# Performance work log

Measured on AMD Instinct MI355X. Metric: run time of the kernel, lower is better.

The kernel has to match this reference:

```python
import jax, jax.numpy as jnp
import numpy as np

B, N, D, H = 8, 1024, 1024, 16
DK = D // H


def setup_inputs() -> dict:
    key = jax.random.key(0)
    ks = jax.random.split(key, 5)
    s_in = 1.0 / np.sqrt(D)
    return {
        "x": jax.random.normal(ks[0], (B, N, D), dtype=jnp.float32),
        "w_qkv": jax.random.uniform(ks[1], (D, 3 * D), jnp.float32, -s_in, s_in),
        "b_qkv": jax.random.uniform(ks[2], (3 * D,), jnp.float32, -s_in, s_in),
        "w_proj": jax.random.uniform(ks[3], (D, D), jnp.float32, -s_in, s_in),
        "b_proj": jax.random.uniform(ks[4], (D,), jnp.float32, -s_in, s_in),
    }


def reference(x, w_qkv, b_qkv, w_proj, b_proj):
    # x: (B, N, D)
    qkv = x @ w_qkv + b_qkv                      # (B, N, 3D)
    q, k, v = jnp.split(qkv, 3, axis=-1)
    # reshape to (B, H, N, DK)
    def heads(t):
        return t.reshape(B, N, H, DK).transpose(0, 2, 1, 3)
    q, k, v = heads(q), heads(k), heads(v)
    scale = 1.0 / np.sqrt(DK).astype(np.float32)
    scores = jnp.einsum("bhnd,bhmd->bhnm", q, k) * scale  # (B, H, N, N)
    attn = jax.nn.softmax(scores, axis=-1)
    out = jnp.einsum("bhnm,bhmd->bhnd", attn, v)          # (B, H, N, DK)
    out = out.transpose(0, 2, 1, 3).reshape(B, N, D)
    return out @ w_proj + b_proj
```

## Files before the change

### kernel.cpp

```cpp
#include <hip/hip_runtime.h>
#include <hip/hip_bf16.h>


#define BB 8
#define NN 1024
#define DD 1024
#define HH 16
#define DK 64
#define TOK (BB * NN)
#define QKVN (3 * DD)

typedef __attribute__((ext_vector_type(8))) short bf16x8;
typedef __attribute__((ext_vector_type(4))) float f32x4;
typedef __attribute__((ext_vector_type(4))) short short4v;
typedef __attribute__((ext_vector_type(4))) float float4v;

static __device__ __forceinline__ short f2bf(float f) {
  union { float f; unsigned u; } v; v.f = f;
  unsigned r = (v.u + 0x7FFFu + ((v.u >> 16) & 1u)) >> 16;
  return (short)r;
}
static __device__ __forceinline__ short f2bf_rn(float f) {
  __hip_bfloat16 h(f);
  short s;
  __builtin_memcpy(&s, &h, 2);
  return s;
}
static __device__ __forceinline__ float fexp2(float x) {
#if __has_builtin(__builtin_amdgcn_exp2f)
  return __builtin_amdgcn_exp2f(x);
#else
  return __expf(x * 0.69314718056f);
#endif
}

static __device__ __forceinline__ void gload_lds16(const short* g, short* lds, int lane) {
#if __has_builtin(__builtin_amdgcn_global_load_lds)
  __builtin_amdgcn_global_load_lds((const __attribute__((address_space(1))) void*)g,
                                   (__attribute__((address_space(3))) void*)lds, 16, 0, 0);
#else
  ((bf16x8*)lds)[lane] = *(const bf16x8*)g;
#endif
}

static __device__ __forceinline__ void block_barrier() {
  asm volatile("" ::: "memory");
  __builtin_amdgcn_s_barrier();
  asm volatile("" ::: "memory");
}

__global__ __launch_bounds__(256) void cast_f32_bf16(const float* __restrict__ in,
                                                     short* __restrict__ out, long n) {
  long i = ((long)blockIdx.x * blockDim.x + threadIdx.x) * 4;
  if (i >= n) return;
  float4v v = *(const float4v*)(in + i);
  short4v o;
  o[0] = f2bf(v[0]); o[1] = f2bf(v[1]); o[2] = f2bf(v[2]); o[3] = f2bf(v[3]);
  *(short4v*)(out + i) = o;
}

__global__ __launch_bounds__(256) void transpose_cast(const float* __restrict__ in,
                                                      short* __restrict__ out,
                                                      int rows, int cols) {
  __shared__ float tile[32][33];
  int bx = blockIdx.x * 32;
  int by = blockIdx.y * 32;
  int tx = threadIdx.x, ty = threadIdx.y;
#pragma unroll
  for (int q = 0; q < 4; q++)
    tile[ty + 8 * q][tx] = in[(long)(by + ty + 8 * q) * cols + bx + tx];
  __syncthreads();
#pragma unroll
  for (int q = 0; q < 4; q++)
    out[(long)(bx + ty + 8 * q) * rows + by + tx] = f2bf(tile[tx][ty + 8 * q]);
}

__global__ __launch_bounds__(512, 2) void gemm256(const short* __restrict__ A,
                                                  const short* __restrict__ Bt,
                                                  const float* __restrict__ bias,
                                                  short* __restrict__ Cqk,
                                                  short* __restrict__ vT,
                                                  int M, int N, int K, int ldc) {
  __shared__ __align__(16) short lds[2][2][2][128 * 64];
  const int tid = threadIdx.x;
  const int wid = tid >> 6, lane = tid & 63;
  const int r = lane & 15, g = lane >> 4;
  const int wm = wid >> 2, wn = wid & 3;

  const int nwg = gridDim.x * gridDim.y;
  const int flat = blockIdx.y * gridDim.x + blockIdx.x;
  const int swz = (flat & 7) * (nwg >> 3) + (flat >> 3);
  const int bx = swz % gridDim.x, by = swz / gridDim.x;
  const long tileM = (long)by * 256, tileN = (long)bx * 256;

  f32x4 acc[8][4] = {};

  const int sc = ((lane & 7) ^ ((lane >> 3) & 7)) * 8;
  const int srl = lane >> 3;

  const int akc0 = ((0 + g) ^ (r & 7)) * 8;
  const int akc1 = ((4 + g) ^ (r & 7)) * 8;
  const int bn0 = (wn & 1) * 64;
  const int bh = wn >> 1;

#define STAGEA(buf, h, Tt)                                                          \
  {                                                                                 \
    _Pragma("unroll") for (int j = 0; j < 2; j++)                                   \
      gload_lds16(A + (tileM + (h) * 128 + wid * 16 + j * 8 + srl) * (long)K +      \
                      (Tt) * 64 + sc,                                               \
                  &lds[buf][0][h][(wid * 2 + j) * 512], lane);                      \
  }
#define STAGEB(buf, h, Tt)                                                          \
  {                                                                                 \
    _Pragma("unroll") for (int j = 0; j < 2; j++)                                   \
      gload_lds16(Bt + (tileN + (h) * 128 + wid * 16 + j * 8 + srl) * (long)K +     \
                      (Tt) * 64 + sc,                                               \
                  &lds[buf][1][h][(wid * 2 + j) * 512], lane);                      \
  }
#define READ_A(q, p)                                                                \
  af[0][0] = *(const bf16x8*)&lds[q][0][wm][((p) * 32 + r) * 64 + akc0];            \
  af[0][1] = *(const bf16x8*)&lds[q][0][wm][((p) * 32 + r) * 64 + akc1];            \
  af[1][0] = *(const bf16x8*)&lds[q][0][wm][((p) * 32 + 16 + r) * 64 + akc0];       \
  af[1][1] = *(const bf16x8*)&lds[q][0][wm][((p) * 32 + 16 + r) * 64 + akc1];
#define READ_B(q)                                                                   \
  {                                                                                 \
    const short* Bh = &lds[q][1][bh][0];                                            \
    _Pragma("unroll") for (int fn = 0; fn < 4; fn++) {                              \
      bf[fn][0] = *(const bf16x8*)&Bh[(bn0 + fn * 16 + r) * 64 + akc0];             \
      bf[fn][1] = *(const bf16x8*)&Bh[(bn0 + fn * 16 + r) * 64 + akc1];             \
    }                                                                               \
  }
#define MFMA_P(p)                                                                   \
  __builtin_amdgcn_s_setprio(1);                                                    \
  _Pragma("unroll") for (int fmi = 0; fmi < 2; fmi++)                               \
      _Pragma("unroll") for (int fn = 0; fn < 4; fn++) {                            \
    acc[2 * (p) + fmi][fn] = __builtin_amdgcn_mfma_f32_16x16x32_bf16(               \
        af[fmi][0], bf[fn][0], acc[2 * (p) + fmi][fn], 0, 0, 0);                    \
    acc[2 * (p) + fmi][fn] = __builtin_amdgcn_mfma_f32_16x16x32_bf16(               \
        af[fmi][1], bf[fn][1], acc[2 * (p) + fmi][fn], 0, 0, 0);                    \
  }                                                                                 \
  __builtin_amdgcn_s_setprio(0);

  const int NT = K >> 6;
  const int NIT = NT >> 1;

  STAGEA(0, 0, 0); STAGEA(0, 1, 0); STAGEB(0, 0, 0); STAGEB(0, 1, 0);
  STAGEB(1, 0, 1); STAGEB(1, 1, 1);
  asm volatile("s_waitcnt vmcnt(4)" ::: "memory");
  block_barrier();

  for (int i = 0; i < NIT; ++i) {
    const int t1 = 2 * i + 1, t2 = 2 * i + 2, t3 = 2 * i + 3;
    const bool full = (i < NIT - 1);
    bf16x8 af[2][2], bf[4][2];

    READ_A(0, 0); READ_B(0);
    STAGEA(1, 0, t1);
    block_barrier(); MFMA_P(0); block_barrier();

    READ_A(0, 1);
    STAGEA(1, 1, t1);
    block_barrier(); MFMA_P(1); block_barrier();

    READ_A(0, 2);
    if (full) STAGEB(0, 0, t2);
    block_barrier(); MFMA_P(2); block_barrier();

    READ_A(0, 3);
    if (full) STAGEB(0, 1, t2);
    if (full) asm volatile("s_waitcnt vmcnt(4)" ::: "memory");
    else      asm volatile("s_waitcnt vmcnt(0)" ::: "memory");
    block_barrier(); MFMA_P(3); block_barrier();

    READ_A(1, 0); READ_B(1);
    if (full) STAGEA(0, 0, t2);
    block_barrier(); MFMA_P(0); block_barrier();

    READ_A(1, 1);
    if (full) STAGEA(0, 1, t2);
    block_barrier(); MFMA_P(1); block_barrier();

    READ_A(1, 2);
    if (full) STAGEB(1, 0, t3);
    block_barrier(); MFMA_P(2); block_barrier();

    READ_A(1, 3);
    if (full) STAGEB(1, 1, t3);
    if (full) asm volatile("s_waitcnt vmcnt(4)" ::: "memory");
    block_barrier(); MFMA_P(3); block_barrier();
  }
#undef STAGEA
#undef STAGEB
#undef READ_A
#undef READ_B
#undef MFMA_P

#pragma unroll
  for (int fm = 0; fm < 8; fm++) {
    long rowb = tileM + wm * 128 + fm * 16 + g * 4;
#pragma unroll
    for (int fn = 0; fn < 4; fn++) {
      long cn = tileN + wn * 64 + fn * 16 + r;
      float bv = bias[cn];
      float v0 = acc[fm][fn][0] + bv;
      float v1 = acc[fm][fn][1] + bv;
      float v2 = acc[fm][fn][2] + bv;
      float v3 = acc[fm][fn][3] + bv;
      if (cn < 2048) {
        Cqk[(rowb + 0) * ldc + cn] = f2bf(v0);
        Cqk[(rowb + 1) * ldc + cn] = f2bf(v1);
        Cqk[(rowb + 2) * ldc + cn] = f2bf(v2);
        Cqk[(rowb + 3) * ldc + cn] = f2bf(v3);
      } else {
        int hc = (int)(cn - 2048);
        int b = (int)(rowb >> 10);
        int n0 = (int)(rowb & 1023);
        int pos = (n0 & ~31) + 8 * ((n0 >> 2) & 3) + 4 * ((n0 >> 4) & 1);
        long va = ((long)(b * 16 + (hc >> 6)) * 64 + (hc & 63)) * 1024 + pos;
        short4v sv;
        sv[0] = f2bf(v0); sv[1] = f2bf(v1); sv[2] = f2bf(v2); sv[3] = f2bf(v3);
        *(short4v*)&vT[va] = sv;
      }
    }
  }
}

template <int MODE>
__global__ __launch_bounds__(256) void gemm_bt(const short* __restrict__ A,
                                               const short* __restrict__ Bt,
                                               const float* __restrict__ bias,
                                               void* __restrict__ Cout,
                                               short* __restrict__ vT,
                                               int M, int N, int K, int ldc) {
  __shared__ __align__(16) short As[2][128 * 32];
  __shared__ __align__(16) short Bs[2][128 * 32];
  const int tid = threadIdx.x;
  const int w = tid >> 6, lane = tid & 63;
  const int r = lane & 15, g = lane >> 4;
  const int wm = w >> 1, wn = w & 1;

  const int nwg = gridDim.x * gridDim.y;
  const int flat = blockIdx.y * gridDim.x + blockIdx.x;
  const int swz = (flat & 7) * (nwg >> 3) + (flat >> 3);
  const int bx = swz % gridDim.x, by = swz / gridDim.x;

  const long tileM = (long)by * 128;
  const long tileN = (long)bx * 128;

  f32x4 acc[4][4] = {};

  const int rowInChunk = lane >> 2;
  const int colOff = ((lane & 3) ^ ((lane >> 3) & 3)) * 8;
  const int rdChunk = (g ^ ((r >> 1) & 3)) * 8;

  const int nt = K >> 5;
#pragma unroll
  for (int issue = 0; issue < 2; ++issue) {
    int c = w * 2 + issue;
    gload_lds16(A + (tileM + c * 16 + rowInChunk) * (long)K + colOff, &As[0][c * 512], lane);
    gload_lds16(Bt + (tileN + c * 16 + rowInChunk) * (long)K + colOff, &Bs[0][c * 512], lane);
  }
  __syncthreads();

  for (int t = 0; t < nt; ++t) {
    const int cur = t & 1;
    if (t + 1 < nt) {
      const int k0 = (t + 1) << 5;
#pragma unroll
      for (int issue = 0; issue < 2; ++issue) {
        int c = w * 2 + issue;
        gload_lds16(A + (tileM + c * 16 + rowInChunk) * (long)K + k0 + colOff,
                    &As[cur ^ 1][c * 512], lane);
        gload_lds16(Bt + (tileN + c * 16 + rowInChunk) * (long)K + k0 + colOff,
                    &Bs[cur ^ 1][c * 512], lane);
      }
    }

    bf16x8 a[4], b[4];
#pragma unroll
    for (int i = 0; i < 4; i++)
      a[i] = *(const bf16x8*)&As[cur][(wm * 64 + i * 16 + r) * 32 + rdChunk];
#pragma unroll
    for (int i = 0; i < 4; i++)
      b[i] = *(const bf16x8*)&Bs[cur][(wn * 64 + i * 16 + r) * 32 + rdChunk];
#pragma unroll
    for (int i = 0; i < 4; i++)
#pragma unroll
      for (int ii = 0; ii < 4; ii++)
        acc[i][ii] = __builtin_amdgcn_mfma_f32_16x16x32_bf16(a[i], b[ii], acc[i][ii], 0, 0, 0);

    __syncthreads();
  }

#pragma unroll
  for (int i = 0; i < 4; i++) {
    long rowb = tileM + wm * 64 + i * 16 + g * 4;
#pragma unroll
    for (int ii = 0; ii < 4; ii++) {
      long cn = tileN + wn * 64 + ii * 16 + r;
      float bv = bias[cn];
      float v0 = acc[i][ii][0] + bv;
      float v1 = acc[i][ii][1] + bv;
      float v2 = acc[i][ii][2] + bv;
      float v3 = acc[i][ii][3] + bv;
      if constexpr (MODE == 0) {
        float* C = (float*)Cout;
        C[(rowb + 0) * ldc + cn] = v0;
        C[(rowb + 1) * ldc + cn] = v1;
        C[(rowb + 2) * ldc + cn] = v2;
        C[(rowb + 3) * ldc + cn] = v3;
      } else {
        short* C = (short*)Cout;
        C[(rowb + 0) * ldc + cn] = f2bf(v0);
        C[(rowb + 1) * ldc + cn] = f2bf(v1);
        C[(rowb + 2) * ldc + cn] = f2bf(v2);
        C[(rowb + 3) * ldc + cn] = f2bf(v3);
      }
    }
  }
}

__global__ __launch_bounds__(256) void attn_kernel(const short* __restrict__ qk,
                                                   const short* __restrict__ vT,
                                                   short* __restrict__ attn_out) {
  __shared__ __align__(16) short Ks[64 * 64];
  __shared__ __align__(16) short Vs[64 * 64];

  const int nwg = gridDim.x * gridDim.y;
  const int flat = blockIdx.y * gridDim.x + blockIdx.x;
  const int swz = (flat & 7) * (nwg >> 3) + (flat >> 3);
  const int bh = swz >> 3;
  const int qt = swz & 7;

  const int bb = bh >> 4, h = bh & 15;
  const int tid = threadIdx.x;
  const int wid = tid >> 6, lane = tid & 63;
  const int r = lane & 15, g = lane >> 4;
  const int qbase = qt * 128 + wid * 32;
  const int RS = 2048;
  const long base = (long)bb * NN * RS;
  const short* Qp = qk + base + h * 64;
  const short* Kp = qk + base + DD + h * 64;
  const short* vTh = vT + (long)bh * 64 * 1024;

  const int srow0 = 8 * wid + (lane >> 3);
  const int sj = (lane & 7) ^ (lane >> 3);

  bf16x8 qf[2][2];
#pragma unroll
  for (int qg = 0; qg < 2; qg++) {
    const short* qrow = Qp + (long)(qbase + 16 * qg + r) * RS;
    qf[qg][0] = *(const bf16x8*)(qrow + 8 * g);
    qf[qg][1] = *(const bf16x8*)(qrow + 32 + 8 * g);
  }

  const float C = 0.18033688f;
  float m2[2] = {-3e38f, -3e38f}, lsum[2] = {0.0f, 0.0f};
  f32x4 o[2][4] = {};

  for (int kv0 = 0; kv0 < NN; kv0 += 64) {
    __syncthreads();
#pragma unroll
    for (int i = 0; i < 2; i++) {
      int srow = 32 * i + srow0;
      gload_lds16(Kp + (long)(kv0 + srow) * RS + sj * 8, &Ks[i * 2048 + wid * 512], lane);
      gload_lds16(vTh + (long)srow * 1024 + kv0 + sj * 8, &Vs[i * 2048 + wid * 512], lane);
    }
    __syncthreads();

    bf16x8 kf[2][2][2];
#pragma unroll
    for (int c = 0; c < 2; c++)
#pragma unroll
      for (int u = 0; u < 2; u++) {
        int krow = 32 * c + 16 * u + r;
#pragma unroll
        for (int s = 0; s < 2; s++)
          kf[c][u][s] = *(const bf16x8*)&Ks[krow * 64 + (((4 * s + g) ^ (r & 7)) * 8)];
      }

    bf16x8 pf[2][2];
#pragma unroll
    for (int qg = 0; qg < 2; qg++) {
      f32x4 s[2][2];
      __builtin_amdgcn_s_setprio(1);
#pragma unroll
      for (int c = 0; c < 2; c++)
#pragma unroll
        for (int u = 0; u < 2; u++) {
          f32x4 t = {};
          t = __builtin_amdgcn_mfma_f32_16x16x32_bf16(kf[c][u][0], qf[qg][0], t, 0, 0, 0);
          s[c][u] = __builtin_amdgcn_mfma_f32_16x16x32_bf16(kf[c][u][1], qf[qg][1], t, 0, 0, 0);
        }
      __builtin_amdgcn_s_setprio(0);

      float s16[16];
#pragma unroll
      for (int c = 0; c < 2; c++)
#pragma unroll
        for (int j = 0; j < 4; j++) {
          s16[8 * c + j] = s[c][0][j];
          s16[8 * c + 4 + j] = s[c][1][j];
        }

      float t8[8];
#pragma unroll
      for (int j = 0; j < 8; j++) t8[j] = fmaxf(s16[j], s16[j + 8]);
#pragma unroll
      for (int j = 0; j < 4; j++) t8[j] = fmaxf(t8[j], t8[j + 4]);
      float tmax = fmaxf(fmaxf(t8[0], t8[1]), fmaxf(t8[2], t8[3]));
      tmax = fmaxf(tmax, __shfl_xor(tmax, 16));
      tmax = fmaxf(tmax, __shfl_xor(tmax, 32));
      float tm2 = tmax * C;

      if (!__all(tm2 <= m2[qg] + 11.5416f)) {
        float mnew = fmaxf(m2[qg], tm2);
        float corr = fexp2(m2[qg] - mnew);
#pragma unroll
        for (int t = 0; t < 4; t++)
#pragma unroll
          for (int j = 0; j < 4; j++) o[qg][t][j] *= corr;
        lsum[qg] *= corr;
        m2[qg] = mnew;
      }

      float pv[16];
#pragma unroll
      for (int j = 0; j < 16; j++) pv[j] = fexp2(fmaf(s16[j], C, -m2[qg]));
      float s8[8];
#pragma unroll
      for (int j = 0; j < 8; j++) s8[j] = pv[j] + pv[j + 8];
#pragma unroll
      for (int j = 0; j < 4; j++) s8[j] = s8[j] + s8[j + 4];
      float ps = (s8[0] + s8[1]) + (s8[2] + s8[3]);
      ps += __shfl_xor(ps, 16);
      ps += __shfl_xor(ps, 32);
      lsum[qg] += ps;
#pragma unroll
      for (int c = 0; c < 2; c++)
#pragma unroll
        for (int j = 0; j < 8; j++) pf[qg][c][j] = f2bf_rn(pv[8 * c + j]);
    }

#pragma unroll
    for (int t = 0; t < 4; t++) {
      int vrow = 16 * t + r;
#pragma unroll
      for (int c = 0; c < 2; c++) {
        bf16x8 vt = *(const bf16x8*)&Vs[vrow * 64 + (((4 * c + g) ^ (r & 7)) * 8)];
        __builtin_amdgcn_s_setprio(1);
        o[0][t] = __builtin_amdgcn_mfma_f32_16x16x32_bf16(vt, pf[0][c], o[0][t], 0, 0, 0);
        o[1][t] = __builtin_amdgcn_mfma_f32_16x16x32_bf16(vt, pf[1][c], o[1][t], 0, 0, 0);
        __builtin_amdgcn_s_setprio(0);
      }
    }
  }

#pragma unroll
  for (int qg = 0; qg < 2; qg++) {
    float inv = 1.0f / lsum[qg];
    long orow = (long)(bb * NN + qbase + 16 * qg + r) * DD + h * 64;
#pragma unroll
    for (int t = 0; t < 4; t++) {
      short4v svv;
#pragma unroll
      for (int j = 0; j < 4; j++) svv[j] = f2bf(o[qg][t][j] * inv);
      *(short4v*)&attn_out[orow + 16 * t + 4 * g] = svv;
    }
  }
}

extern "C" void kernel_launch(void* const* d_in, const int* in_sizes, int n_in,
                              void* d_out, int out_size, void* d_ws, size_t ws_size,
                              hipStream_t stream) {
  const float* x = (const float*)d_in[0];
  const float* w_qkv = (const float*)d_in[1];
  const float* b_qkv = (const float*)d_in[2];
  const float* w_proj = (const float*)d_in[3];
  const float* b_proj = (const float*)d_in[4];
  float* out = (float*)d_out;

  short* ws = (short*)d_ws;
  short* xb = ws;
  short* wqkvT = xb + (long)TOK * DD;
  short* wprojT = wqkvT + (long)QKVN * DD;
  short* qkb = wprojT + (long)DD * DD;
  short* vT = qkb + (long)TOK * 2048;
  short* attn = vT + (long)TOK * DD;

  cast_f32_bf16<<<(TOK * DD) / (256 * 4), 256, 0, stream>>>(x, xb, (long)TOK * DD);
  transpose_cast<<<dim3(QKVN / 32, DD / 32), dim3(32, 8), 0, stream>>>(w_qkv, wqkvT, DD, QKVN);
  transpose_cast<<<dim3(DD / 32, DD / 32), dim3(32, 8), 0, stream>>>(w_proj, wprojT, DD, DD);

  gemm256<<<dim3(QKVN / 256, TOK / 256), 512, 0, stream>>>(xb, wqkvT, b_qkv, qkb, vT,
                                                           TOK, QKVN, DD, 2048);

  attn_kernel<<<dim3(8, BB * HH), 256, 0, stream>>>(qkb, vT, attn);

  gemm_bt<0><<<dim3(DD / 128, TOK / 128), 256, 0, stream>>>(attn, wprojT, b_proj, out, nullptr,
                                                            TOK, DD, DD, DD);
}
```

Baseline: 180.1 us.

## Split V projection into separate GEMM and add LDS waits before MFMA phases

```diff
diff --git a/kernel.cpp b/kernel.cpp
--- a/kernel.cpp
+++ b/kernel.cpp
@@ -79,7 +79,6 @@
                                                   const short* __restrict__ Bt,
                                                   const float* __restrict__ bias,
                                                   short* __restrict__ Cqk,
-                                                  short* __restrict__ vT,
                                                   int M, int N, int K, int ldc) {
   __shared__ __align__(16) short lds[2][2][2][128 * 64];
   const int tid = threadIdx.x;
@@ -101,7 +100,7 @@
   const int akc0 = ((0 + g) ^ (r & 7)) * 8;
   const int akc1 = ((4 + g) ^ (r & 7)) * 8;
   const int bn0 = (wn & 1) * 64;
-  const int bh = wn >> 1;
+  const int bhh = wn >> 1;
 
 #define STAGEA(buf, h, Tt)                                                          \
   {                                                                                 \
@@ -124,12 +123,15 @@
   af[1][1] = *(const bf16x8*)&lds[q][0][wm][((p) * 32 + 16 + r) * 64 + akc1];
 #define READ_B(q)                                                                   \
   {                                                                                 \
-    const short* Bh = &lds[q][1][bh][0];                                            \
+    const short* Bh = &lds[q][1][bhh][0];                                           \
     _Pragma("unroll") for (int fn = 0; fn < 4; fn++) {                              \
       bf[fn][0] = *(const bf16x8*)&Bh[(bn0 + fn * 16 + r) * 64 + akc0];             \
       bf[fn][1] = *(const bf16x8*)&Bh[(bn0 + fn * 16 + r) * 64 + akc1];             \
     }                                                                               \
   }
+#define WAITL()                                                                     \
+  asm volatile("s_waitcnt lgkmcnt(0)" ::: "memory");                                \
+  __builtin_amdgcn_sched_barrier(0);
 #define MFMA_P(p)                                                                   \
   __builtin_amdgcn_s_setprio(1);                                                    \
   _Pragma("unroll") for (int fmi = 0; fmi < 2; fmi++)                               \
@@ -156,43 +158,44 @@
 
     READ_A(0, 0); READ_B(0);
     STAGEA(1, 0, t1);
-    block_barrier(); MFMA_P(0); block_barrier();
+    block_barrier(); WAITL(); MFMA_P(0); block_barrier();
 
     READ_A(0, 1);
     STAGEA(1, 1, t1);
-    block_barrier(); MFMA_P(1); block_barrier();
+    block_barrier(); WAITL(); MFMA_P(1); block_barrier();
 
     READ_A(0, 2);
     if (full) STAGEB(0, 0, t2);
-    block_barrier(); MFMA_P(2); block_barrier();
+    block_barrier(); WAITL(); MFMA_P(2); block_barrier();
 
     READ_A(0, 3);
     if (full) STAGEB(0, 1, t2);
     if (full) asm volatile("s_waitcnt vmcnt(4)" ::: "memory");
     else      asm volatile("s_waitcnt vmcnt(0)" ::: "memory");
-    block_barrier(); MFMA_P(3); block_barrier();
+    block_barrier(); WAITL(); MFMA_P(3); block_barrier();
 
     READ_A(1, 0); READ_B(1);
     if (full) STAGEA(0, 0, t2);
-    block_barrier(); MFMA_P(0); block_barrier();
+    block_barrier(); WAITL(); MFMA_P(0); block_barrier();
 
     READ_A(1, 1);
     if (full) STAGEA(0, 1, t2);
-    block_barrier(); MFMA_P(1); block_barrier();
+    block_barrier(); WAITL(); MFMA_P(1); block_barrier();
 
     READ_A(1, 2);
     if (full) STAGEB(1, 0, t3);
-    block_barrier(); MFMA_P(2); block_barrier();
+    block_barrier(); WAITL(); MFMA_P(2); block_barrier();
 
     READ_A(1, 3);
     if (full) STAGEB(1, 1, t3);
     if (full) asm volatile("s_waitcnt vmcnt(4)" ::: "memory");
-    block_barrier(); MFMA_P(3); block_barrier();
+    block_barrier(); WAITL(); MFMA_P(3); block_barrier();
   }
 #undef STAGEA
 #undef STAGEB
 #undef READ_A
 #undef READ_B
+#undef WAITL
 #undef MFMA_P
 
 #pragma unroll
@@ -202,25 +205,10 @@
     for (int fn = 0; fn < 4; fn++) {
       long cn = tileN + wn * 64 + fn * 16 + r;
       float bv = bias[cn];
-      float v0 = acc[fm][fn][0] + bv;
-      float v1 = acc[fm][fn][1] + bv;
-      float v2 = acc[fm][fn][2] + bv;
-      float v3 = acc[fm][fn][3] + bv;
-      if (cn < 2048) {
-        Cqk[(rowb + 0) * ldc + cn] = f2bf(v0);
-        Cqk[(rowb + 1) * ldc + cn] = f2bf(v1);
-        Cqk[(rowb + 2) * ldc + cn] = f2bf(v2);
-        Cqk[(rowb + 3) * ldc + cn] = f2bf(v3);
-      } else {
-        int hc = (int)(cn - 2048);
-        int b = (int)(rowb >> 10);
-        int n0 = (int)(rowb & 1023);
-        int pos = (n0 & ~31) + 8 * ((n0 >> 2) & 3) + 4 * ((n0 >> 4) & 1);
-        long va = ((long)(b * 16 + (hc >> 6)) * 64 + (hc & 63)) * 1024 + pos;
-        short4v sv;
-        sv[0] = f2bf(v0); sv[1] = f2bf(v1); sv[2] = f2bf(v2); sv[3] = f2bf(v3);
-        *(short4v*)&vT[va] = sv;
-      }
+      Cqk[(rowb + 0) * ldc + cn] = f2bf(acc[fm][fn][0] + bv);
+      Cqk[(rowb + 1) * ldc + cn] = f2bf(acc[fm][fn][1] + bv);
+      Cqk[(rowb + 2) * ldc + cn] = f2bf(acc[fm][fn][2] + bv);
+      Cqk[(rowb + 3) * ldc + cn] = f2bf(acc[fm][fn][3] + bv);
     }
   }
 }
@@ -310,11 +298,14 @@
         C[(rowb + 2) * ldc + cn] = v2;
         C[(rowb + 3) * ldc + cn] = v3;
       } else {
-        short* C = (short*)Cout;
-        C[(rowb + 0) * ldc + cn] = f2bf(v0);
-        C[(rowb + 1) * ldc + cn] = f2bf(v1);
-        C[(rowb + 2) * ldc + cn] = f2bf(v2);
-        C[(rowb + 3) * ldc + cn] = f2bf(v3);
+        int hc = (int)cn;
+        int b = (int)(rowb >> 10);
+        int n0 = (int)(rowb & 1023);
+        int pos = (n0 & ~31) + 8 * ((n0 >> 2) & 3) + 4 * ((n0 >> 4) & 1);
+        long va = ((long)(b * 16 + (hc >> 6)) * 64 + (hc & 63)) * 1024 + pos;
+        short4v sv;
+        sv[0] = f2bf(v0); sv[1] = f2bf(v1); sv[2] = f2bf(v2); sv[3] = f2bf(v3);
+        *(short4v*)&vT[va] = sv;
       }
     }
   }
@@ -492,8 +483,11 @@
   transpose_cast<<<dim3(QKVN / 32, DD / 32), dim3(32, 8), 0, stream>>>(w_qkv, wqkvT, DD, QKVN);
   transpose_cast<<<dim3(DD / 32, DD / 32), dim3(32, 8), 0, stream>>>(w_proj, wprojT, DD, DD);
 
-  gemm256<<<dim3(QKVN / 256, TOK / 256), 512, 0, stream>>>(xb, wqkvT, b_qkv, qkb, vT,
-                                                           TOK, QKVN, DD, 2048);
+  gemm256<<<dim3(2048 / 256, TOK / 256), 512, 0, stream>>>(xb, wqkvT, b_qkv, qkb,
+                                                           TOK, 2048, DD, 2048);
+
+  gemm_bt<2><<<dim3(DD / 128, TOK / 128), 256, 0, stream>>>(
+      xb, wqkvT + (long)2048 * DD, b_qkv + 2048, nullptr, vT, TOK, DD, DD, 0);
 
   attn_kernel<<<dim3(8, BB * HH), 256, 0, stream>>>(qkb, vT, attn);
 
```

After: 176.6 us. No clear change (-1.9%).
